# Optimization experiments

Measured on AMD Instinct MI355X. Metric: run time of the kernel, lower is better.

The kernel has to match this reference:

```python
import jax, jax.numpy as jnp
import numpy as np

BATCH = 8
NUM_CLASSES = 80
COF_DIM = 128  # num_basic_masks(32) * sub_region_x(2) * sub_region_y(2)
STRIDES = (8, 16, 32)
SIZES = ((100, 152), (50, 76), (25, 38))
IMG_H, IMG_W = 800, 1216
PRE_NMS_THRESH = 0.05
PRE_NMS_TOP_N = 1000
NMS_THRESH = 0.6
POST_NMS_TOP_N = 100
THRESH_WITH_CTR = False
CLASS_OFFSET = float(max(IMG_H, IMG_W) + 1)  # batched_nms class-offset trick


def _make_locations(h, w, stride):
    xs = jnp.arange(w, dtype=jnp.float32) * stride + stride // 2
    ys = jnp.arange(h, dtype=jnp.float32) * stride + stride // 2
    Y, X = jnp.meshgrid(ys, xs, indexing='ij')
    return jnp.stack([X.reshape(-1), Y.reshape(-1)], axis=-1)  # [HW,2] (x,y)


def setup_inputs() -> dict:
    key = jax.random.key(0)
    inp = {}
    for i, ((h, w), s) in enumerate(zip(SIZES, STRIDES)):
        k1, k2, k3, k4, key = jax.random.split(key, 5)
        inp[f'locations{i}'] = _make_locations(h, w, s)
        # shift logits down so the pre_nms threshold actually prunes some candidates
        inp[f'logits{i}'] = jax.random.normal(k1, (BATCH, NUM_CLASSES, h, w), jnp.float32) - 2.0
        inp[f'reg{i}'] = jax.random.uniform(k2, (BATCH, 4, h, w), jnp.float32, minval=0.5, maxval=8.0)
        inp[f'ctr{i}'] = jax.random.normal(k3, (BATCH, 1, h, w), jnp.float32)
        inp[f'cofs{i}'] = jax.random.normal(k4, (BATCH, COF_DIM, h, w), jnp.float32)
    return inp


def _level(locs, logits, reg, ctr, cofs, stride):
    # faithful port of forward_for_single_feature_map, fixed-size (padded) version
    N, C, H, W = logits.shape
    HW = H * W
    K = PRE_NMS_TOP_N
    scores = jax.nn.sigmoid(logits).transpose(0, 2, 3, 1).reshape(N, HW, C)
    reg = reg.transpose(0, 2, 3, 1).reshape(N, HW, 4) * stride
    ctr = jax.nn.sigmoid(ctr.reshape(N, HW))
    cofs = cofs.transpose(0, 2, 3, 1).reshape(N, HW, -1)
    if THRESH_WITH_CTR:
        scores = scores * ctr[:, :, None]
    cand = scores > PRE_NMS_THRESH
    if not THRESH_WITH_CTR:
        scores = scores * ctr[:, :, None]
    flat = jnp.where(cand, scores, -1.0).reshape(N, HW * C)
    n_cand = jnp.minimum(cand.reshape(N, -1).sum(-1), K)  # per-image pre_nms_top_n clamp
    vals, idx = jax.lax.top_k(flat, K)
    valid = jnp.arange(K)[None, :] < n_cand[:, None]
    loc_idx = idx // C
    cls = idx % C
    pl = locs[loc_idx]                                        # [N,K,2]
    pr = jnp.take_along_axis(reg, loc_idx[..., None], axis=1)  # [N,K,4]
    pc = jnp.take_along_axis(cofs, loc_idx[..., None], axis=1) # [N,K,COF_DIM]
    x1 = jnp.clip(pl[..., 0] - pr[..., 0], 0.0, IMG_W)
    y1 = jnp.clip(pl[..., 1] - pr[..., 1], 0.0, IMG_H)
    x2 = jnp.clip(pl[..., 0] + pr[..., 2], 0.0, IMG_W)
    y2 = jnp.clip(pl[..., 1] + pr[..., 3], 0.0, IMG_H)
    boxes = jnp.stack([x1, y1, x2, y2], axis=-1)
    return boxes, vals, cls, pc, valid


def _pairwise_iou(b):
    area = (b[:, 2] - b[:, 0]) * (b[:, 3] - b[:, 1])
    lt = jnp.maximum(b[:, None, :2], b[None, :, :2])
    rb = jnp.minimum(b[:, None, 2:], b[None, :, 2:])
    wh = jnp.clip(rb - lt, 0.0, None)
    inter = wh[..., 0] * wh[..., 1]
    return inter / (area[:, None] + area[None, :] - inter + 1e-9)


def _nms_single(boxes, scores, classes, cofs, valid):
    # ml_nms / batched_nms: class-offset boxes, greedy suppression, keep top post_nms_top_n
    K = boxes.shape[0]
    s = jnp.where(valid, scores, -1.0)
    order = jnp.argsort(-s)
    b = boxes[order]
    sv = s[order]
    c = classes[order]
    pc = cofs[order]
    v = valid[order]
    ob = b + (c.astype(b.dtype) * CLASS_OFFSET)[:, None]
    sup = _pairwise_iou(ob) > NMS_THRESH
    idxs = jnp.arange(K)
    def body(i, keep):
        return keep & ~(keep[i] & sup[i] & (idxs > i))
    keep = jax.lax.fori_loop(0, K, body, v)
    final = jnp.where(keep, sv, -1.0)
    _, topi = jax.lax.top_k(final, POST_NMS_TOP_N)
    kv = keep[topi]
    out_boxes = jnp.where(kv[:, None], b[topi], 0.0)
    # FCOS/SipMask reports sqrt(cls_score * ctrness)
    out_scores = jnp.where(kv, jnp.sqrt(jnp.maximum(sv[topi], 1e-12)), 0.0)
    out_cls = jnp.where(kv, c[topi], -1)
    out_cofs = jnp.where(kv[:, None], pc[topi], 0.0)
    return out_boxes, out_scores, out_cls, out_cofs, kv


def reference(locations0, logits0, reg0, ctr0, cofs0,
              locations1, logits1, reg1, ctr1, cofs1,
              locations2, logits2, reg2, ctr2, cofs2):
    levels = [(locations0, logits0, reg0, ctr0, cofs0),
              (locations1, logits1, reg1, ctr1, cofs1),
              (locations2, logits2, reg2, ctr2, cofs2)]
    outs = [_level(*lv, s) for lv, s in zip(levels, STRIDES)]
    boxes = jnp.concatenate([o[0] for o in outs], axis=1)
    scores = jnp.concatenate([o[1] for o in outs], axis=1)
    classes = jnp.concatenate([o[2] for o in outs], axis=1)
    cofs = jnp.concatenate([o[3] for o in outs], axis=1)
    valid = jnp.concatenate([o[4] for o in outs], axis=1)
    return jax.vmap(_nms_single)(boxes, scores, classes, cofs, valid)
```

## Files before the change

kernel.cpp:

```cpp
#include <hip/hip_runtime.h>

typedef unsigned int u32;
typedef unsigned long long u64;
typedef float vf4 __attribute__((ext_vector_type(4)));

#define NCLS 80
#define NIMG 8
#define PRE_K 1000
#define POST_K 100
#define PBUF_N 2048

__device__ __forceinline__ int HWof(int l){ return l==0?15200:(l==1?3800:950); }
__device__ __forceinline__ float STRof(int l){ return l==0?8.f:(l==1?16.f:32.f); }
__device__ __forceinline__ u32 CAPof(int l){ return l==0?65536u:32768u; }
__device__ __forceinline__ u32 POFFof(int l){ return l==0?0u:(l==1?65536u:98304u); }

struct Ptrs {
  const float* logits[3];
  const float* reg[3];
  const float* ctr[3];
  const float* cofs[3];
  const float* locs[3];
};

#define NB0 149
#define NB1 38
#define NBALL 197

#define OFF_PCNT  0u
#define OFF_CAND  128u
#define OFF_MCNT  256u
#define OFF_KEEP  320u
#define ZERO_BYTES 3392u
#define OFF_THR   3392u
#define OFF_POOL  4224u
#define OFF_SORT  8392832u
#define OFF_CLS   8589440u
#define OFF_MERG  8687744u

__device__ __forceinline__ float sigmoidf(float x){ return 1.0f/(1.0f+expf(-x)); }

template<int LVL>
__device__ __forceinline__ void collect_body(int tile, int img, const Ptrs& p,
                                             u32* cand, u32* pcnt, u64* pool,
                                             u64* pbuf, u32* shctl){
  constexpr int HW   = LVL==0?15200:(LVL==1?3800:950);
  constexpr int NE   = 80*HW;
  constexpr int NF4  = NE/4;
  const u32 CAP = CAPof(LVL);
  const int pair = img*3 + LVL;
  const size_t poff = (size_t)img*131072u + POFFof(LVL);
  const u32 tbin = (LVL==0?501u:(LVL==1?500u:496u));
  const float marg = (LVL==0? -0.7895f : (LVL==1? -1.0996f : -1.9470f));
  const vf4* plane = (const vf4*)(p.logits[LVL] + (size_t)img*NE);
  const float* cptr = p.ctr[LVL] + (size_t)img*HW;
  if (threadIdx.x==0){ shctl[0]=0; shctl[1]=0; }
  __syncthreads();
  vf4 vv[8], cc[8];
  #pragma unroll
  for (int k=0;k<8;++k){
    int f4 = tile*2048 + k*256 + (int)threadIdx.x;
    int cf = f4 < NF4 ? f4 : NF4-1;
    vv[k] = plane[cf];
    int e0 = cf*4;
    if (LVL==2){
      vf4 c;
      #pragma unroll
      for (int j=0;j<4;++j){ int e=e0+j; int cl=e/HW; c[j]=cptr[e-cl*HW]; }
      cc[k]=c;
    } else {
      int loc0 = e0 - (e0/HW)*HW;
      cc[k] = *(const vf4*)(cptr + loc0);
    }
  }
  asm volatile("" : "+v"(vv[0]),"+v"(vv[1]),"+v"(vv[2]),"+v"(vv[3]),
                    "+v"(vv[4]),"+v"(vv[5]),"+v"(vv[6]),"+v"(vv[7]),
                    "+v"(cc[0]),"+v"(cc[1]),"+v"(cc[2]),"+v"(cc[3]),
                    "+v"(cc[4]),"+v"(cc[5]),"+v"(cc[6]),"+v"(cc[7]));
  u32 mc = 0;
  #pragma unroll
  for (int k=0;k<8;++k){
    int f4 = tile*2048 + k*256 + (int)threadIdx.x;
    if (f4 < NF4){
      int e0 = f4*4;
      int cls0 = e0 / HW;
      int loc0 = e0 - cls0*HW;
      #pragma unroll
      for (int j=0;j<4;++j){
        float x = vv[k][j];
        if (x > -2.94443898f) mc++;
        if (x > marg){
          float sl = sigmoidf(x);
          float sc = sigmoidf(cc[k][j]);
          u32 bits = __float_as_uint(sl * sc);
          if ((bits>>21) >= tbin){
            int e = e0 + j, cls, loc;
            if (LVL==2){ cls=e/HW; loc=e-cls*HW; } else { cls=cls0; loc=loc0+j; }
            u64 key = ((u64)bits<<32) | (u64)(0xFFFFFFFFu - (u32)(loc*NCLS + cls));
            u32 id = atomicAdd(&shctl[0], 1u);
            if (id < (u32)PBUF_N) pbuf[id] = key;
            else { u32 g = atomicAdd(&pcnt[pair],1u); if (g<CAP) pool[poff+g]=key; }
          }
        }
      }
    }
  }
  if (mc) atomicAdd(&shctl[1], mc);
  __syncthreads();
  u32 m = shctl[0]; if (m > (u32)PBUF_N) m = PBUF_N;
  if (threadIdx.x==0){
    if (m) shctl[2] = atomicAdd(&pcnt[pair], m);
    if (shctl[1]) atomicAdd(&cand[pair], shctl[1]);
  }
  __syncthreads();
  for (u32 i=threadIdx.x; i<m; i+=256){
    u32 d = shctl[2] + i;
    if (d < CAP) pool[poff+d] = pbuf[i];
  }
}

__global__ __launch_bounds__(256)
void fused_pass(Ptrs p, u32* cand, u32* pcnt, u64* pool){
  __shared__ u64 pbuf[PBUF_N];
  __shared__ u32 shctl[4];
  const int bx=(int)blockIdx.x, img=(int)blockIdx.y;
  if (bx<NB0)          collect_body<0>(bx,        img,p,cand,pcnt,pool,pbuf,shctl);
  else if (bx<NB0+NB1) collect_body<1>(bx-NB0,    img,p,cand,pcnt,pool,pbuf,shctl);
  else                 collect_body<2>(bx-NB0-NB1,img,p,cand,pcnt,pool,pbuf,shctl);
}

template<int LVL>
__device__ __forceinline__ void slow_hist(const Ptrs& p, int img, u32* h){
  constexpr int HW = LVL==0?15200:(LVL==1?3800:950);
  constexpr int NE = 80*HW, NF4 = NE/4;
  const vf4* plane = (const vf4*)(p.logits[LVL] + (size_t)img*NE);
  const float* cptr = p.ctr[LVL] + (size_t)img*HW;
  for (int f4=(int)threadIdx.x; f4<NF4; f4+=1024){
    vf4 v = plane[f4];
    int e0=f4*4;
    #pragma unroll
    for (int j=0;j<4;++j){
      float sl=sigmoidf(v[j]);
      if (sl>0.05f){
        int e=e0+j; int c=e/HW; int loc=e-c*HW;
        u32 bits=__float_as_uint(sl*sigmoidf(cptr[loc]));
        atomicAdd(&h[bits>>21],1u);
      }
    }
  }
}
template<int LVL>
__device__ __forceinline__ void slow_refill(const Ptrs& p, int img, u32 B1,
                                            u64* pool, size_t poff, u32* cnt){
  constexpr int HW = LVL==0?15200:(LVL==1?3800:950);
  constexpr int NE = 80*HW, NF4 = NE/4;
  const u32 CAP = CAPof(LVL);
  const vf4* plane = (const vf4*)(p.logits[LVL] + (size_t)img*NE);
  const float* cptr = p.ctr[LVL] + (size_t)img*HW;
  for (int f4=(int)threadIdx.x; f4<NF4; f4+=1024){
    vf4 v = plane[f4];
    int e0=f4*4;
    #pragma unroll
    for (int j=0;j<4;++j){
      float sl=sigmoidf(v[j]);
      if (sl>0.05f){
        int e=e0+j; int c=e/HW; int loc=e-c*HW;
        u32 bits=__float_as_uint(sl*sigmoidf(cptr[loc]));
        if ((bits>>21) >= B1){
          u32 id = atomicAdd(cnt,1u);
          if (id<CAP) pool[poff+id] = ((u64)bits<<32) |
                        (u64)(0xFFFFFFFFu - (u32)(loc*NCLS + c));
        }
      }
    }
  }
}

__global__ __launch_bounds__(1024)
void selsort(Ptrs p, const u32* cand, const u32* pcnt, u32* thr,
             u64* pool, u64* sorted){
  const int pair=(int)blockIdx.x, lvl=pair%3, img=pair/3;
  const int tid=(int)threadIdx.x;
  __shared__ u64 a[2048];
  __shared__ u32 h[512];
  __shared__ u32 h2[2048];
  __shared__ u32 seg[256], exc[256];
  __shared__ u32 sB1, sCnt, sT22, sgc, scnt;
  const size_t poff = (size_t)img*131072u + POFFof(lvl);
  const u32 CAP = CAPof(lvl);
  const u32 kk = min(cand[pair], (u32)PRE_K);
  if (kk==0){ if (tid==0) thr[pair*8+3]=0u; return; }
  const u32 pcRaw = pcnt[pair];
  const bool ok = (pcRaw <= CAP) && (pcRaw >= kk);
  u32 pc = min(pcRaw, CAP);

  for (int b=tid;b<512;b+=1024) h[b]=0;
  __syncthreads();
  if (ok){
    for (u32 i=tid;i<pc;i+=1024) atomicAdd(&h[(u32)(pool[poff+i]>>53)],1u);
  } else {
    if (lvl==0)      slow_hist<0>(p,img,h);
    else if (lvl==1) slow_hist<1>(p,img,h);
    else             slow_hist<2>(p,img,h);
  }
  __syncthreads();
  if (tid<256) seg[tid] = h[511-2*tid] + h[511-(2*tid+1)];
  __syncthreads();
  if (tid==0){ u32 run=0; for(int i=0;i<256;++i){ exc[i]=run; run+=seg[i]; } }
  __syncthreads();
  if (tid<256){
    u32 cum=exc[tid];
    #pragma unroll
    for (int q=0;q<2;++q){
      int bin=511-(2*tid+q); u32 c=h[bin];
      if (c && cum<kk && cum+c>=kk){ sB1=(u32)bin; sCnt=cum; }
      cum+=c;
    }
  }
  __syncthreads();
  const u32 B1=sB1, cntAb=sCnt;
  if (!ok){
    if (tid==0) sgc=0;
    __syncthreads();
    if (lvl==0)      slow_refill<0>(p,img,B1,pool,poff,&sgc);
    else if (lvl==1) slow_refill<1>(p,img,B1,pool,poff,&sgc);
    else             slow_refill<2>(p,img,B1,pool,poff,&sgc);
    __syncthreads();
    pc = min(sgc, CAP);
  }
  for (int b=tid;b<2048;b+=1024) h2[b]=0;
  __syncthreads();
  for (u32 i=tid;i<pc;i+=1024){
    u64 key=pool[poff+i];
    if ((u32)(key>>53)==B1) atomicAdd(&h2[(u32)(key>>42)&0x7FFu],1u);
  }
  __syncthreads();
  const u32 KK2 = kk - cntAb;
  if (tid<256){
    u32 part=0;
    #pragma unroll
    for (int q=0;q<8;++q) part += h2[2047-(tid*8+q)];
    seg[tid]=part;
  }
  __syncthreads();
  if (tid==0){ u32 run=0; for(int i=0;i<256;++i){ exc[i]=run; run+=seg[i]; } }
  __syncthreads();
  if (tid<256){
    u32 cum=exc[tid];
    #pragma unroll
    for (int q=0;q<8;++q){
      int bin=2047-(tid*8+q); u32 c=h2[bin];
      if (c && cum<KK2 && cum+c>=KK2) sT22=(B1<<11)|(u32)bin;
      cum+=c;
    }
  }
  __syncthreads();
  const u32 T22=sT22;
  for (int i=tid;i<2048;i+=1024) a[i]=0ull;
  if (tid==0) scnt=0;
  __syncthreads();
  for (u32 i=tid;i<pc;i+=1024){
    u64 k = pool[poff+i];
    if ((u32)(k>>42) >= T22){
      u32 id = atomicAdd(&scnt,1u);
      if (id < 2048u) a[id]=k;
    }
  }
  __syncthreads();
  const u32 n = min(scnt, 2048u);
  for (int k=2;k<=2048;k<<=1){
    for (int j=k>>1;j>0;j>>=1){
      for (int t=tid;t<2048;t+=1024){
        int ix = t ^ j;
        if (ix > t){
          u64 x=a[t], y=a[ix];
          bool up = ((t & k)==0);
          if (up ? (x<y) : (x>y)){ a[t]=y; a[ix]=x; }
        }
      }
      __syncthreads();
    }
  }
  u32 m = kk < n ? kk : n;
  for (u32 r=tid;r<m;r+=1024) sorted[(size_t)pair*1024+r]=a[r];
  if (tid==0) thr[pair*8+3]=m;
}

__global__ void merge_kernel(Ptrs p, const u32* thr, const u64* sorted,
                             float* merged, float* clsarr, u32* mcnt){
#pragma clang fp contract(off)
  const int img = blockIdx.x;
  __shared__ u64 mk[3][1024];
  __shared__ int n[3];
  if (threadIdx.x < 3) n[threadIdx.x] = (int)thr[(img*3+threadIdx.x)*8+3];
  __syncthreads();
  const int n0=n[0], n1=n[1], n2=n[2];
  for (int idx=threadIdx.x; idx<3*1024; idx+=blockDim.x){
    int l = idx>>10, r = idx&1023;
    if (r < n[l]){
      u64 key = sorted[(size_t)(img*3+l)*1024 + r];
      mk[l][r] = (key & 0xFFFFFFFF00000000ull) |
                 (u64)(0xFFFFFFFFu - (u32)(l*PRE_K + r));
    }
  }
  __syncthreads();
  const int T = n0+n1+n2;
  if (threadIdx.x==0) mcnt[img] = (u32)T;
  for (int t=threadIdx.x; t<T; t+=blockDim.x){
    int l, r;
    if (t < n0){ l=0; r=t; }
    else if (t < n0+n1){ l=1; r=t-n0; }
    else { l=2; r=t-n0-n1; }
    u64 x = mk[l][r];
    int pos = r;
    #pragma unroll
    for (int o=0;o<3;++o) if (o!=l){
      int lo=0, hi=n[o];
      while (lo<hi){ int m=(lo+hi)>>1; if (mk[o][m] > x) lo=m+1; else hi=m; }
      pos += lo;
    }
    u64 key = sorted[(size_t)(img*3+l)*1024 + r];
    u32 flat = 0xFFFFFFFFu - (u32)(key & 0xFFFFFFFFull);
    float score = __uint_as_float((u32)(key>>32));
    int HW = HWof(l);
    int loc = (int)(flat / (u32)NCLS);
    int cls = (int)(flat - (u32)loc*NCLS);
    float lx = p.locs[l][2*loc], ly = p.locs[l][2*loc+1];
    float st = STRof(l);
    const float* rg = p.reg[l] + (size_t)img*4*HW + loc;
    float r0 = rg[0]*st, r1 = rg[HW]*st, r2 = rg[2*(size_t)HW]*st, r3 = rg[3*(size_t)HW]*st;
    float x1 = fminf(fmaxf(lx - r0, 0.f), 1216.f);
    float y1 = fminf(fmaxf(ly - r1, 0.f),  800.f);
    float x2 = fminf(fmaxf(lx + r2, 0.f), 1216.f);
    float y2 = fminf(fmaxf(ly + r3, 0.f),  800.f);
    float* out = merged + (size_t)(img*3072 + pos)*8;
    out[0]=x1; out[1]=y1; out[2]=x2; out[3]=y2;
    out[4]=score; out[5]=(float)cls; out[6]=(float)l; out[7]=(float)loc;
    clsarr[img*3072 + pos] = (float)cls;
  }
}

__global__ __launch_bounds__(64)
void nms_class(const float* merged_all, const float* clsarr, const u32* mcnt, u64* gkeep){
#pragma clang fp contract(off)
  const int c = (int)blockIdx.x, img = (int)blockIdx.y;
  const float* merged = merged_all + (size_t)img*3072*8;
  const float* carr = clsarr + (size_t)img*3072;
  const int T = (int)mcnt[img];
  const int lane = (int)threadIdx.x;
  __shared__ unsigned short mlist[3072];
  __shared__ float4 kbox[1024];

  float fv[48];
  #pragma unroll
  for (int w=0; w<48; ++w){
    int j = w*64 + lane;
    fv[w] = (j < T) ? carr[j] : -1.0f;
  }
  int base = 0;
  const u64 lanemask = (lane==0) ? 0ull : ((~0ull) >> (64-lane));
  #pragma unroll
  for (int w=0; w<48; ++w){
    bool mem = ((int)fv[w] == c);
    u64 word = __ballot(mem);
    if (mem){
      int rank = base + (int)__popcll(word & lanemask);
      mlist[rank] = (unsigned short)(w*64 + lane);
    }
    base += (int)__popcll(word);
  }
  const int n = base;
  if (n == 0) return;
  __syncthreads();

  const float off = (float)c * 1217.0f;
  int kc = 0;
  for (int t0 = 0; t0 < n; t0 += 64){
    int r = t0 + lane;
    bool valid = (r < n);
    float4 bx = make_float4(0.f,0.f,0.f,0.f);
    int gj = 0;
    if (valid){
      gj = (int)mlist[r];
      const float* rec = merged + (size_t)gj*8;
      bx = make_float4(rec[0]+off, rec[1]+off, rec[2]+off, rec[3]+off);
    }
    float ax = (bx.z-bx.x)*(bx.w-bx.y);
    bool alive_l = valid;
    for (int q=0; q<kc; ++q){
      float4 bq = kbox[q];
      float aq = (bq.z-bq.x)*(bq.w-bq.y);
      float ltx=fmaxf(bq.x,bx.x), lty=fmaxf(bq.y,bx.y);
      float rbx=fminf(bq.z,bx.z), rby=fminf(bq.w,bx.w);
      float wx=fmaxf(rbx-ltx,0.f), wy=fmaxf(rby-lty,0.f);
      float inter=wx*wy;
      float denom=aq+ax; denom=denom-inter; denom=denom+1e-9f;
      if (alive_l && (inter/denom > 0.6f)) alive_l=false;
    }
    u64 alive = __ballot(alive_l);
    while (alive){
      int i = __ffsll((unsigned long long)alive) - 1;
      float bix=__shfl(bx.x,i), biy=__shfl(bx.y,i), biz=__shfl(bx.z,i), biw=__shfl(bx.w,i);
      int gi = __shfl(gj, i);
      if (lane==0){
        atomicOr((unsigned long long*)&gkeep[img*48 + (gi>>6)], 1ull<<(gi&63));
        if (kc < 1024) kbox[kc] = make_float4(bix,biy,biz,biw);
      }
      kc++;
      float ai=(biz-bix)*(biw-biy);
      float ltx=fmaxf(bix,bx.x), lty=fmaxf(biy,bx.y);
      float rbx=fminf(biz,bx.z), rby=fminf(biw,bx.w);
      float wx=fmaxf(rbx-ltx,0.f), wy=fmaxf(rby-lty,0.f);
      float inter=wx*wy;
      float denom=ai+ax; denom=denom-inter; denom=denom+1e-9f;
      bool supp = alive_l && (inter/denom > 0.6f);
      u64 killm = __ballot(supp);
      alive &= ~killm;
      alive &= ~(1ull<<i);
      alive_l = alive_l && !supp;
    }
    __syncthreads();
  }
}

__global__ __launch_bounds__(128)
void emit_kernel(Ptrs p, const float* merged_all, const u64* gkeep, float* out){
  const int r = (int)blockIdx.x, img = (int)blockIdx.y;
  const int tid = (int)threadIdx.x;
  __shared__ int s_i, s_kept;
  if (tid < 64){
    u64 word = (tid < 48) ? gkeep[img*48 + tid] : 0ull;
    int c = (int)__popcll(word);
    int inc = c;
    #pragma unroll
    for (int d=1; d<64; d<<=1){
      int y = __shfl_up(inc, d);
      if (tid >= d) inc += y;
    }
    int excl = inc - c;
    int total = __shfl(inc, 63);
    int kept = total < POST_K ? total : POST_K;
    if (tid==0){ s_kept = kept; s_i = -1; }
    bool sel = (tid<48) && (r < kept) && (excl <= r) && (r < excl + c);
    if (sel){
      u64 w = word; int need = r - excl;
      for (int q=0;q<need;++q) w &= w-1ull;
      s_i = (tid<<6) + (int)__ffsll((unsigned long long)w) - 1;
    }
  }
  __syncthreads();
  const int i = s_i; const int kept = s_kept;
  const bool has = (r < kept) && (i >= 0);
  const float* rec = merged_all + (size_t)img*3072*8 + (size_t)(has?i:0)*8;
  float* obx = out;
  float* osc = out + 3200;
  float* ocl = out + 4000;
  float* ocf = out + 4800;
  float* okv = out + 107200;
  if (tid==0) osc[img*POST_K+r] = has ? sqrtf(fmaxf(rec[4], 1e-12f)) : 0.f;
  if (tid==1) ocl[img*POST_K+r] = has ? rec[5] : -1.0f;
  if (tid==2) okv[img*POST_K+r] = has ? 1.0f : 0.f;
  if (tid>=4 && tid<8) obx[(img*POST_K+r)*4 + (tid-4)] = has ? rec[tid-4] : 0.f;
  float v = 0.f;
  if (has){
    int l = (int)rec[6]; int loc = (int)rec[7];
    int HW = HWof(l);
    v = p.cofs[l][((size_t)img*128 + tid)*HW + loc];
  }
  ocf[(img*POST_K + r)*128 + tid] = v;
}

extern "C" void kernel_launch(void* const* d_in, const int* in_sizes, int n_in,
                              void* d_out, int out_size, void* d_ws, size_t ws_size,
                              hipStream_t stream){
  Ptrs p;
  for (int l=0; l<3; ++l){
    p.locs[l]   = (const float*)d_in[5*l+0];
    p.logits[l] = (const float*)d_in[5*l+1];
    p.reg[l]    = (const float*)d_in[5*l+2];
    p.ctr[l]    = (const float*)d_in[5*l+3];
    p.cofs[l]   = (const float*)d_in[5*l+4];
  }
  char* ws = (char*)d_ws;
  u32* pcnt   = (u32*)(ws + OFF_PCNT);
  u32* cand   = (u32*)(ws + OFF_CAND);
  u32* mcnt   = (u32*)(ws + OFF_MCNT);
  u64* gkeep  = (u64*)(ws + OFF_KEEP);
  u32* thr    = (u32*)(ws + OFF_THR);
  u64* pool   = (u64*)(ws + OFF_POOL);
  u64* sorted = (u64*)(ws + OFF_SORT);
  float* clsarr = (float*)(ws + OFF_CLS);
  float* merged = (float*)(ws + OFF_MERG);

  hipMemsetAsync(ws, 0, ZERO_BYTES, stream);
  fused_pass<<<dim3(NBALL,8), 256, 0, stream>>>(p, cand, pcnt, pool);
  selsort<<<24, 1024, 0, stream>>>(p, cand, pcnt, thr, pool, sorted);
  merge_kernel<<<8, 1024, 0, stream>>>(p, thr, sorted, merged, clsarr, mcnt);
  nms_class<<<dim3(NCLS,8), 64, 0, stream>>>(merged, clsarr, mcnt, gkeep);
  emit_kernel<<<dim3(POST_K,8), 128, 0, stream>>>(p, merged, gkeep, (float*)d_out);
}
```

Baseline: 163.6 us.

## Fuse level merge into per-class NMS kernel, removing merge_kernel launch

Drops the separate merge kernel. Each per-class NMS block now loads the three per-level sorted key lists into shared memory and picks out its own class members. It computes their global merged rank by binary search, bitonic-sorts those members by rank, and decodes boxes on the fly. Only kept boxes are written to the merged buffer. This saves one launch plus the global round trip of merged/class arrays, at the cost of redundant shared-memory loads and binary searches in every one of the 640 small blocks.

Result: slower. 257.8 us (+57.6%).

```diff
diff --git a/kernel.cpp b/kernel.cpp
--- a/kernel.cpp
+++ b/kernel.cpp
@@ -29,14 +29,12 @@
 
 #define OFF_PCNT  0u
 #define OFF_CAND  128u
-#define OFF_MCNT  256u
-#define OFF_KEEP  320u
-#define ZERO_BYTES 3392u
-#define OFF_THR   3392u
-#define OFF_POOL  4224u
-#define OFF_SORT  8392832u
-#define OFF_CLS   8589440u
-#define OFF_MERG  8687744u
+#define OFF_KEEP  256u
+#define ZERO_BYTES 3328u
+#define OFF_THR   3328u
+#define OFF_POOL  4096u
+#define OFF_SORT  8392704u
+#define OFF_MERG  8589312u
 
 __device__ __forceinline__ float sigmoidf(float x){ return 1.0f/(1.0f+expf(-x)); }
 
@@ -286,104 +284,100 @@
   if (tid==0) thr[pair*8+3]=m;
 }
 
-__global__ void merge_kernel(Ptrs p, const u32* thr, const u64* sorted,
-                             float* merged, float* clsarr, u32* mcnt){
-#pragma clang fp contract(off)
-  const int img = blockIdx.x;
-  __shared__ u64 mk[3][1024];
-  __shared__ int n[3];
-  if (threadIdx.x < 3) n[threadIdx.x] = (int)thr[(img*3+threadIdx.x)*8+3];
-  __syncthreads();
-  const int n0=n[0], n1=n[1], n2=n[2];
-  for (int idx=threadIdx.x; idx<3*1024; idx+=blockDim.x){
-    int l = idx>>10, r = idx&1023;
-    if (r < n[l]){
-      u64 key = sorted[(size_t)(img*3+l)*1024 + r];
-      mk[l][r] = (key & 0xFFFFFFFF00000000ull) |
-                 (u64)(0xFFFFFFFFu - (u32)(l*PRE_K + r));
-    }
-  }
-  __syncthreads();
-  const int T = n0+n1+n2;
-  if (threadIdx.x==0) mcnt[img] = (u32)T;
-  for (int t=threadIdx.x; t<T; t+=blockDim.x){
-    int l, r;
-    if (t < n0){ l=0; r=t; }
-    else if (t < n0+n1){ l=1; r=t-n0; }
-    else { l=2; r=t-n0-n1; }
-    u64 x = mk[l][r];
-    int pos = r;
-    #pragma unroll
-    for (int o=0;o<3;++o) if (o!=l){
-      int lo=0, hi=n[o];
-      while (lo<hi){ int m=(lo+hi)>>1; if (mk[o][m] > x) lo=m+1; else hi=m; }
-      pos += lo;
-    }
-    u64 key = sorted[(size_t)(img*3+l)*1024 + r];
-    u32 flat = 0xFFFFFFFFu - (u32)(key & 0xFFFFFFFFull);
-    float score = __uint_as_float((u32)(key>>32));
-    int HW = HWof(l);
-    int loc = (int)(flat / (u32)NCLS);
-    int cls = (int)(flat - (u32)loc*NCLS);
-    float lx = p.locs[l][2*loc], ly = p.locs[l][2*loc+1];
-    float st = STRof(l);
-    const float* rg = p.reg[l] + (size_t)img*4*HW + loc;
-    float r0 = rg[0]*st, r1 = rg[HW]*st, r2 = rg[2*(size_t)HW]*st, r3 = rg[3*(size_t)HW]*st;
-    float x1 = fminf(fmaxf(lx - r0, 0.f), 1216.f);
-    float y1 = fminf(fmaxf(ly - r1, 0.f),  800.f);
-    float x2 = fminf(fmaxf(lx + r2, 0.f), 1216.f);
-    float y2 = fminf(fmaxf(ly + r3, 0.f),  800.f);
-    float* out = merged + (size_t)(img*3072 + pos)*8;
-    out[0]=x1; out[1]=y1; out[2]=x2; out[3]=y2;
-    out[4]=score; out[5]=(float)cls; out[6]=(float)l; out[7]=(float)loc;
-    clsarr[img*3072 + pos] = (float)cls;
-  }
-}
-
 __global__ __launch_bounds__(64)
-void nms_class(const float* merged_all, const float* clsarr, const u32* mcnt, u64* gkeep){
+void nms_class(Ptrs p, const u32* thr, const u64* sorted_all,
+               u64* gkeep, float* merged_all){
 #pragma clang fp contract(off)
   const int c = (int)blockIdx.x, img = (int)blockIdx.y;
-  const float* merged = merged_all + (size_t)img*3072*8;
-  const float* carr = clsarr + (size_t)img*3072;
-  const int T = (int)mcnt[img];
   const int lane = (int)threadIdx.x;
-  __shared__ unsigned short mlist[3072];
+  __shared__ u64 lv[3][1024];
+  __shared__ u32 mem[4096];
   __shared__ float4 kbox[1024];
-
-  float fv[48];
-  #pragma unroll
-  for (int w=0; w<48; ++w){
-    int j = w*64 + lane;
-    fv[w] = (j < T) ? carr[j] : -1.0f;
-  }
-  int base = 0;
-  const u64 lanemask = (lane==0) ? 0ull : ((~0ull) >> (64-lane));
-  #pragma unroll
-  for (int w=0; w<48; ++w){
-    bool mem = ((int)fv[w] == c);
-    u64 word = __ballot(mem);
-    if (mem){
-      int rank = base + (int)__popcll(word & lanemask);
-      mlist[rank] = (unsigned short)(w*64 + lane);
-    }
-    base += (int)__popcll(word);
-  }
-  const int n = base;
+  __shared__ int sn[3];
+  if (lane < 3) sn[lane] = (int)thr[(img*3+lane)*8+3];
+  __syncthreads();
+  for (int i=lane; i<3*1024; i+=64){
+    int l = i>>10, r = i&1023;
+    lv[l][r] = (r < sn[l]) ? sorted_all[(size_t)(img*3+l)*1024 + r] : 0ull;
+  }
+  __syncthreads();
+  const u64 lanemask = (lane==0)?0ull:((~0ull)>>(64-lane));
+  u32 base = 0;
+  for (int l=0;l<3;++l){
+    const int nl = sn[l];
+    for (int t0=0;t0<nl;t0+=64){
+      int r = t0+lane;
+      bool ismem = false;
+      u32 pos = 0;
+      if (r < nl){
+        u64 key = lv[l][r];
+        u32 flat = 0xFFFFFFFFu - (u32)key;
+        if ((int)(flat % (u32)NCLS) == c){
+          ismem = true;
+          u32 bits = (u32)(key>>32);
+          pos = (u32)r;
+          #pragma unroll
+          for (int o=0;o<3;++o) if (o!=l){
+            int lo=0, hi=sn[o];
+            if (o<l){ while (lo<hi){ int m=(lo+hi)>>1; if ((u32)(lv[o][m]>>32) >= bits) lo=m+1; else hi=m; } }
+            else    { while (lo<hi){ int m=(lo+hi)>>1; if ((u32)(lv[o][m]>>32) >  bits) lo=m+1; else hi=m; } }
+            pos += (u32)lo;
+          }
+        }
+      }
+      u64 word = __ballot(ismem);
+      if (ismem){
+        u32 rank = base + (u32)__popcll(word & lanemask);
+        mem[rank] = (pos<<12) | ((u32)l<<10) | (u32)r;
+      }
+      base += (u32)__popcll(word);
+    }
+  }
+  const int n = (int)base;
   if (n == 0) return;
   __syncthreads();
-
+  int np2 = 64; while (np2 < n) np2 <<= 1;
+  for (int i=lane+n; i<np2; i+=64) mem[i] = 0xFFFFFFFFu;
+  __syncthreads();
+  for (int k=2;k<=np2;k<<=1){
+    for (int j=k>>1;j>0;j>>=1){
+      for (int t=lane;t<np2;t+=64){
+        int ix = t^j;
+        if (ix>t){
+          u32 x=mem[t], y=mem[ix];
+          bool up = ((t&k)==0);
+          if (up ? (x>y) : (x<y)){ mem[t]=y; mem[ix]=x; }
+        }
+      }
+      __syncthreads();
+    }
+  }
   const float off = (float)c * 1217.0f;
+  float* merged = merged_all + (size_t)img*3072*8;
   int kc = 0;
-  for (int t0 = 0; t0 < n; t0 += 64){
-    int r = t0 + lane;
-    bool valid = (r < n);
+  for (int t0=0;t0<n;t0+=64){
+    int r = t0+lane;
+    bool valid = (r<n);
     float4 bx = make_float4(0.f,0.f,0.f,0.f);
-    int gj = 0;
+    float u0=0.f,u1=0.f,u2=0.f,u3=0.f, score=0.f;
+    int loc=0, ml=0, ppos=0;
     if (valid){
-      gj = (int)mlist[r];
-      const float* rec = merged + (size_t)gj*8;
-      bx = make_float4(rec[0]+off, rec[1]+off, rec[2]+off, rec[3]+off);
+      u32 m = mem[r];
+      ppos = (int)(m>>12); ml=(int)((m>>10)&3u); int rr=(int)(m&1023u);
+      u64 key = lv[ml][rr];
+      u32 flat = 0xFFFFFFFFu - (u32)key;
+      score = __uint_as_float((u32)(key>>32));
+      loc = (int)(flat/(u32)NCLS);
+      int HW = HWof(ml);
+      float lx = p.locs[ml][2*loc], ly = p.locs[ml][2*loc+1];
+      float st = STRof(ml);
+      const float* rg = p.reg[ml] + (size_t)img*4*HW + loc;
+      float r0 = rg[0]*st, r1v = rg[HW]*st, r2 = rg[2*(size_t)HW]*st, r3 = rg[3*(size_t)HW]*st;
+      u0 = fminf(fmaxf(lx - r0, 0.f), 1216.f);
+      u1 = fminf(fmaxf(ly - r1v, 0.f),  800.f);
+      u2 = fminf(fmaxf(lx + r2, 0.f), 1216.f);
+      u3 = fminf(fmaxf(ly + r3, 0.f),  800.f);
+      bx = make_float4(u0+off, u1+off, u2+off, u3+off);
     }
     float ax = (bx.z-bx.x)*(bx.w-bx.y);
     bool alive_l = valid;
@@ -400,10 +394,15 @@
     u64 alive = __ballot(alive_l);
     while (alive){
       int i = __ffsll((unsigned long long)alive) - 1;
-      float bix=__shfl(bx.x,i), biy=__shfl(bx.y,i), biz=__shfl(bx.z,i), biw=__shfl(bx.w,i);
-      int gi = __shfl(gj, i);
+      float kx0=__shfl(u0,i), ky0=__shfl(u1,i), kx1=__shfl(u2,i), ky1=__shfl(u3,i);
+      float ks=__shfl(score,i);
+      int   kloc=__shfl(loc,i), kl=__shfl(ml,i), kpos=__shfl(ppos,i);
+      float bix=kx0+off, biy=ky0+off, biz=kx1+off, biw=ky1+off;
       if (lane==0){
-        atomicOr((unsigned long long*)&gkeep[img*48 + (gi>>6)], 1ull<<(gi&63));
+        atomicOr((unsigned long long*)&gkeep[img*48 + (kpos>>6)], 1ull<<(kpos&63));
+        float* o = merged + (size_t)kpos*8;
+        o[0]=kx0; o[1]=ky0; o[2]=kx1; o[3]=ky1;
+        o[4]=ks; o[5]=(float)c; o[6]=(float)kl; o[7]=(float)kloc;
         if (kc < 1024) kbox[kc] = make_float4(bix,biy,biz,biw);
       }
       kc++;
@@ -484,18 +483,15 @@
   char* ws = (char*)d_ws;
   u32* pcnt   = (u32*)(ws + OFF_PCNT);
   u32* cand   = (u32*)(ws + OFF_CAND);
-  u32* mcnt   = (u32*)(ws + OFF_MCNT);
   u64* gkeep  = (u64*)(ws + OFF_KEEP);
   u32* thr    = (u32*)(ws + OFF_THR);
   u64* pool   = (u64*)(ws + OFF_POOL);
   u64* sorted = (u64*)(ws + OFF_SORT);
-  float* clsarr = (float*)(ws + OFF_CLS);
   float* merged = (float*)(ws + OFF_MERG);
 
   hipMemsetAsync(ws, 0, ZERO_BYTES, stream);
   fused_pass<<<dim3(NBALL,8), 256, 0, stream>>>(p, cand, pcnt, pool);
   selsort<<<24, 1024, 0, stream>>>(p, cand, pcnt, thr, pool, sorted);
-  merge_kernel<<<8, 1024, 0, stream>>>(p, thr, sorted, merged, clsarr, mcnt);
-  nms_class<<<dim3(NCLS,8), 64, 0, stream>>>(merged, clsarr, mcnt, gkeep);
+  nms_class<<<dim3(NCLS,8), 64, 0, stream>>>(p, thr, sorted, gkeep, merged);
   emit_kernel<<<dim3(POST_K,8), 128, 0, stream>>>(p, merged, gkeep, (float*)d_out);
 }
```
